# Optimization experiments

Hardware: AMD Instinct MI355X
Metric: run time of the kernel (lower is better)

The kernel has to match this reference:

```python
import jax, jax.numpy as jnp
import numpy as np

B, S, H = 2, 2048, 2048
NH = 16
Q_LORA = 1536
KV_LORA = 512
NOPE = 128
ROPE = 64
QHD = NOPE + ROPE  # 192
VHD = 128
FF = 8192
EPS = 1e-6
THETA = 10000.0


def rmsnorm(x, w, eps=EPS):
    var = jnp.mean(jnp.square(x), axis=-1, keepdims=True)
    return w * (x * jax.lax.rsqrt(var + eps))


def rotate_half(x):
    x1 = x[..., : x.shape[-1] // 2]
    x2 = x[..., x.shape[-1] // 2 :]
    return jnp.concatenate((-x2, x1), axis=-1)


def _deinterleave(x):
    # torch: x.view(b,h,s,d//2,2).transpose(0,1,2,4,3).reshape(b,h,s,d)
    b, h, s, d = x.shape
    return x.reshape(b, h, s, d // 2, 2).transpose(0, 1, 2, 4, 3).reshape(b, h, s, d)


def setup_inputs() -> dict:
    key = jax.random.key(0)
    ks = jax.random.split(key, 16)
    sc = 0.02
    # RoPE tables [S, ROPE]
    inv_freq = 1.0 / (THETA ** (np.arange(0, ROPE, 2, dtype=np.float64) / ROPE))
    freqs = np.outer(np.arange(S, dtype=np.float64), inv_freq)
    emb = np.concatenate([freqs, freqs], axis=-1)
    pos = jnp.sort(jax.random.randint(ks[15], (B, S), 0, S), axis=-1)
    return {
        "hidden_states": jax.random.normal(ks[0], (B, S, H), jnp.float32),
        "ln1_w": jnp.ones((H,), jnp.float32),
        "q_a_kernel": jax.random.normal(ks[1], (H, Q_LORA), jnp.float32) * sc,
        "q_a_ln_w": jnp.ones((Q_LORA,), jnp.float32),
        "q_b_kernel": jax.random.normal(ks[2], (Q_LORA, NH * QHD), jnp.float32) * sc,
        "kv_a_kernel": jax.random.normal(ks[3], (H, KV_LORA + ROPE), jnp.float32) * sc,
        "kv_a_ln_w": jnp.ones((KV_LORA,), jnp.float32),
        "kv_b_kernel": jax.random.normal(ks[4], (KV_LORA, NH * (NOPE + VHD)), jnp.float32) * sc,
        "o_kernel": jax.random.normal(ks[5], (NH * VHD, H), jnp.float32) * sc,
        "ln2_w": jnp.ones((H,), jnp.float32),
        "gate_kernel": jax.random.normal(ks[6], (H, FF), jnp.float32) * sc,
        "up_kernel": jax.random.normal(ks[7], (H, FF), jnp.float32) * sc,
        "down_kernel": jax.random.normal(ks[8], (FF, H), jnp.float32) * sc,
        "sin": jnp.asarray(np.sin(emb), jnp.float32),
        "cos": jnp.asarray(np.cos(emb), jnp.float32),
        "position_ids": pos,
    }


def reference(hidden_states, ln1_w, q_a_kernel, q_a_ln_w, q_b_kernel,
              kv_a_kernel, kv_a_ln_w, kv_b_kernel, o_kernel, ln2_w,
              gate_kernel, up_kernel, down_kernel, sin, cos, position_ids):
    b, s, h = hidden_states.shape
    x = rmsnorm(hidden_states, ln1_w)

    # --- MLA attention ---
    q = rmsnorm(x @ q_a_kernel, q_a_ln_w) @ q_b_kernel        # [b,s,NH*QHD]
    q = q.reshape(b, s, NH, QHD).transpose(0, 2, 1, 3)        # [b,NH,s,QHD]
    q_nope, q_pe = q[..., :NOPE], q[..., NOPE:]

    ckv = x @ kv_a_kernel                                     # [b,s,KV_LORA+ROPE]
    k_pe = ckv[..., KV_LORA:].reshape(b, s, 1, ROPE).transpose(0, 2, 1, 3)  # [b,1,s,ROPE]
    kv = rmsnorm(ckv[..., :KV_LORA], kv_a_ln_w) @ kv_b_kernel
    kv = kv.reshape(b, s, NH, NOPE + VHD).transpose(0, 2, 1, 3)
    k_nope = kv[..., :NOPE]
    v = kv[..., NOPE:]                                        # [b,NH,s,VHD]

    cos_e = cos[position_ids][:, None]                        # [b,1,s,ROPE]
    sin_e = sin[position_ids][:, None]
    q_pe = _deinterleave(q_pe)
    k_pe = _deinterleave(k_pe)
    q_pe = q_pe * cos_e + rotate_half(q_pe) * sin_e
    k_pe = k_pe * cos_e + rotate_half(k_pe) * sin_e

    qs = jnp.concatenate([q_nope, q_pe], axis=-1)             # [b,NH,s,QHD]
    ks = jnp.concatenate([k_nope, jnp.broadcast_to(k_pe, (b, NH, s, ROPE))], axis=-1)

    scale = QHD ** -0.5
    scores = jnp.einsum("bhqd,bhkd->bhqk", qs, ks) * scale
    causal = jnp.tril(jnp.ones((s, s), dtype=bool))
    scores = jnp.where(causal, scores, jnp.finfo(scores.dtype).min)
    probs = jax.nn.softmax(scores, axis=-1)
    attn = jnp.einsum("bhqk,bhkd->bhqd", probs, v)            # [b,NH,s,VHD]
    attn = attn.transpose(0, 2, 1, 3).reshape(b, s, NH * VHD)
    attn_out = attn @ o_kernel

    h1 = hidden_states + attn_out

    # --- dense MLP (SwiGLU) ---
    x2 = rmsnorm(h1, ln2_w)
    mlp = (jax.nn.silu(x2 @ gate_kernel) * (x2 @ up_kernel)) @ down_kernel
    return h1 + mlp
```

## Files before the change

kernel.cpp:

```cpp
#include <hip/hip_runtime.h>
#include <hip/hip_bf16.h>
#include <cstdint>

#define B_ 2
#define S_ 2048
#define H_ 2048
#define NH_ 16
#define QL_ 1536
#define KVL_ 512
#define NOPE_ 128
#define ROPE_ 64
#define QHD_ 192
#define VHD_ 128
#define FF_ 8192
#define BS_ (B_ * S_)
#define CKVP_ 640
#define KVW_ (NOPE_ + VHD_)

typedef __hip_bfloat16 bf16;
typedef __attribute__((ext_vector_type(8))) short short8_t;
typedef __attribute__((ext_vector_type(4))) float f32x4;

__device__ __forceinline__ float ldf(const float* p, size_t i) { return p[i]; }
__device__ __forceinline__ float ldf(const bf16* p, size_t i) { return __bfloat162float(p[i]); }
__device__ __forceinline__ void stf(float* p, size_t i, float v) { p[i] = v; }
__device__ __forceinline__ void stf(bf16* p, size_t i, float v) { p[i] = __float2bfloat16(v); }

__device__ __forceinline__ void gload16(const void* g, void* l)
{
    __builtin_amdgcn_global_load_lds((const unsigned int*)g, (unsigned int*)l, 16, 0, 0);
}

__global__ __launch_bounds__(256) void transp_bf16(
    const float* __restrict__ in, bf16* __restrict__ out, int K, int N, int Npad)
{
    __shared__ float t[32][33];
    const int n0 = blockIdx.x * 32, k0 = blockIdx.y * 32;
    for (int r = threadIdx.y; r < 32; r += 8) {
        const int n = n0 + threadIdx.x;
        t[r][threadIdx.x] = (n < N) ? in[(size_t)(k0 + r) * N + n] : 0.f;
    }
    __syncthreads();
    for (int r = threadIdx.y; r < 32; r += 8) {
        out[(size_t)(n0 + r) * K + k0 + threadIdx.x] = __float2bfloat16(t[threadIdx.x][r]);
    }
}

template<typename InT, typename OutT>
__global__ __launch_bounds__(256) void rmsnorm2(
    const InT* __restrict__ in, const float* __restrict__ w,
    OutT* __restrict__ out, int cols, int istride, int ostride)
{
    const int row = blockIdx.x;
    const InT* ip = in + (size_t)row * istride;
    OutT* op = out + (size_t)row * ostride;

    float ss = 0.f;
    for (int c = threadIdx.x; c < cols; c += 256) {
        float v = ldf(ip, c);
        ss = fmaf(v, v, ss);
    }
    #pragma unroll
    for (int off = 32; off; off >>= 1) ss += __shfl_xor(ss, off);
    __shared__ float red[4];
    if ((threadIdx.x & 63) == 0) red[threadIdx.x >> 6] = ss;
    __syncthreads();
    const float total = red[0] + red[1] + red[2] + red[3];
    const float scale = rsqrtf(total / (float)cols + 1e-6f);
    for (int c = threadIdx.x; c < cols; c += 256) {
        stf(op, c, ldf(ip, c) * scale * w[c]);
    }
}

template<int MODE, typename OutT>
__global__ __launch_bounds__(256) void gemm_bf16(
    const bf16* __restrict__ A, const bf16* __restrict__ BT,
    const float* __restrict__ Df, const bf16* __restrict__ Db,
    OutT* __restrict__ C, int M, int N, int K)
{
    __shared__ short As[128 * 32];
    __shared__ short Bs[128 * 32];
    const int tid = threadIdx.x;
    const int wid = tid >> 6, lane = tid & 63;
    const int bm = blockIdx.y * 128, bn = blockIdx.x * 128;
    const int wr = (wid >> 1) * 64, wc = (wid & 1) * 64;
    const int l16 = lane & 15;
    const int lk = (lane >> 4) << 3;

    f32x4 acc[4][4] = {};

    for (int k0 = 0; k0 < K; k0 += 32) {
        #pragma unroll
        for (int is = 0; is < 2; ++is) {
            const int c = is * 256 + tid;
            const int row = c >> 2;
            const int cb = (c & 3) * 16;
            const char* srcA = (const char*)A + ((size_t)(bm + row) * K + k0) * 2 + cb;
            const char* srcB = (const char*)BT + ((size_t)(bn + row) * K + k0) * 2 + cb;
            char* dstA = (char*)As + (is * 256 + wid * 64) * 16;
            char* dstB = (char*)Bs + (is * 256 + wid * 64) * 16;
            gload16(srcA, dstA);
            gload16(srcB, dstB);
        }
        __syncthreads();

        short8_t a[4], b[4];
        const short* ApW = As + (wr + l16) * 32 + lk;
        const short* BpW = Bs + (wc + l16) * 32 + lk;
        #pragma unroll
        for (int m = 0; m < 4; ++m) a[m] = *(const short8_t*)(ApW + m * 16 * 32);
        #pragma unroll
        for (int n = 0; n < 4; ++n) b[n] = *(const short8_t*)(BpW + n * 16 * 32);
        #pragma unroll
        for (int m = 0; m < 4; ++m)
            #pragma unroll
            for (int n = 0; n < 4; ++n)
                acc[m][n] = __builtin_amdgcn_mfma_f32_16x16x32_bf16(a[m], b[n], acc[m][n], 0, 0, 0);
        __syncthreads();
    }

    const int r0 = bm + wr + ((lane >> 4) << 2);
    const int c0 = bn + wc + l16;
    #pragma unroll
    for (int m = 0; m < 4; ++m) {
        #pragma unroll
        for (int n = 0; n < 4; ++n) {
            const int row = r0 + m * 16;
            const int col = c0 + n * 16;
            #pragma unroll
            for (int r = 0; r < 4; ++r) {
                const size_t off = (size_t)(row + r) * N + col;
                float v = acc[m][n][r];
                if (MODE == 1) v += Df[off];
                if (MODE == 2) {
                    const float g = __bfloat162float(Db[off]);
                    v *= g / (1.f + __expf(-g));
                }
                stf(C, off, v);
            }
        }
    }
}

__device__ __forceinline__ short8_t ldsfrag(const short* half_base, int r, int c)
{
    return *(const short8_t*)(half_base + r * 64 + ((c ^ (r & 7)) << 3));
}

template<int MODE, typename OutT>
__global__ __launch_bounds__(512, 2) void gemm256(
    const bf16* __restrict__ A, const bf16* __restrict__ BT,
    const float* __restrict__ Df, const bf16* __restrict__ Db,
    OutT* __restrict__ C, int M, int N, int K)
{
    __shared__ short lds[2][2][2][128 * 64];

    const int tid = threadIdx.x;
    const int wid = tid >> 6, lane = tid & 63;
    const int wm = wid >> 2, wn = wid & 3;
    const int l16 = lane & 15, hk = lane >> 4;

    const int nwg = gridDim.x * gridDim.y;
    const int orig = blockIdx.y * gridDim.x + blockIdx.x;
    const int q = nwg >> 3, r8 = nwg & 7;
    const int xcd = orig & 7, lid = orig >> 3;
    const int wg = (xcd < r8 ? xcd * (q + 1) : r8 * (q + 1) + (xcd - r8) * q) + lid;
    const int bn = (wg % gridDim.x) * 256;
    const int bm = (wg / gridDim.x) * 256;

    f32x4 acc[8][4] = {};

    const int nt = K >> 6;

    auto stage_half = [&](const bf16* gbase, int ldk, short* lbase) {
        #pragma unroll
        for (int i = 0; i < 2; ++i) {
            const int ch = i * 512 + tid;
            const int row = ch >> 3, pc = ch & 7;
            const int gc = pc ^ (row & 7);
            const char* src = (const char*)(gbase + (size_t)row * ldk + gc * 8);
            char* dst = (char*)lbase + (i * 512 + wid * 64) * 16;
            gload16(src, dst);
        }
    };

    stage_half(A + (size_t)bm * K, K, &lds[0][0][0][0]);
    stage_half(A + (size_t)(bm + 128) * K, K, &lds[0][0][1][0]);
    stage_half(BT + (size_t)bn * K, K, &lds[0][1][0][0]);
    stage_half(BT + (size_t)(bn + 128) * K, K, &lds[0][1][1][0]);
    asm volatile("s_waitcnt vmcnt(0)" ::: "memory");
    __syncthreads();

    int cur = 0;
    for (int t = 0; t < nt; ++t) {
        const int k0n = (t + 1) << 6;
        const short* Ah = &lds[cur][0][wm][0];
        const short* Bh = &lds[cur][1][wn >> 1][0];
        const int brr = (wn & 1) * 64;

        short8_t bfr[4][2], afr[2][2];

        #pragma unroll
        for (int nf = 0; nf < 4; ++nf)
            #pragma unroll
            for (int ks = 0; ks < 2; ++ks)
                bfr[nf][ks] = ldsfrag(Bh, brr + nf * 16 + l16, ks * 4 + hk);
        #pragma unroll
        for (int mi = 0; mi < 2; ++mi)
            #pragma unroll
            for (int ks = 0; ks < 2; ++ks)
                afr[mi][ks] = ldsfrag(Ah, mi * 16 + l16, ks * 4 + hk);
        if (t + 1 < nt) {
            stage_half(A + (size_t)bm * K + k0n, K, &lds[cur ^ 1][0][0][0]);
            stage_half(A + (size_t)(bm + 128) * K + k0n, K, &lds[cur ^ 1][0][1][0]);
        }
        __builtin_amdgcn_s_barrier();
        __builtin_amdgcn_s_setprio(1);
        #pragma unroll
        for (int mi = 0; mi < 2; ++mi)
            #pragma unroll
            for (int nf = 0; nf < 4; ++nf)
                #pragma unroll
                for (int ks = 0; ks < 2; ++ks)
                    acc[mi][nf] = __builtin_amdgcn_mfma_f32_16x16x32_bf16(
                        afr[mi][ks], bfr[nf][ks], acc[mi][nf], 0, 0, 0);
        __builtin_amdgcn_s_setprio(0);
        __builtin_amdgcn_s_barrier();

        #pragma unroll
        for (int mi = 0; mi < 2; ++mi)
            #pragma unroll
            for (int ks = 0; ks < 2; ++ks)
                afr[mi][ks] = ldsfrag(Ah, 32 + mi * 16 + l16, ks * 4 + hk);
        if (t + 1 < nt) {
            stage_half(BT + (size_t)bn * K + k0n, K, &lds[cur ^ 1][1][0][0]);
            stage_half(BT + (size_t)(bn + 128) * K + k0n, K, &lds[cur ^ 1][1][1][0]);
        }
        __builtin_amdgcn_s_barrier();
        __builtin_amdgcn_s_setprio(1);
        #pragma unroll
        for (int mi = 0; mi < 2; ++mi)
            #pragma unroll
            for (int nf = 0; nf < 4; ++nf)
                #pragma unroll
                for (int ks = 0; ks < 2; ++ks)
                    acc[2 + mi][nf] = __builtin_amdgcn_mfma_f32_16x16x32_bf16(
                        afr[mi][ks], bfr[nf][ks], acc[2 + mi][nf], 0, 0, 0);
        __builtin_amdgcn_s_setprio(0);
        __builtin_amdgcn_s_barrier();

        #pragma unroll
        for (int mi = 0; mi < 2; ++mi)
            #pragma unroll
            for (int ks = 0; ks < 2; ++ks)
                afr[mi][ks] = ldsfrag(Ah, 64 + mi * 16 + l16, ks * 4 + hk);
        __builtin_amdgcn_s_barrier();
        __builtin_amdgcn_s_setprio(1);
        #pragma unroll
        for (int mi = 0; mi < 2; ++mi)
            #pragma unroll
            for (int nf = 0; nf < 4; ++nf)
                #pragma unroll
                for (int ks = 0; ks < 2; ++ks)
                    acc[4 + mi][nf] = __builtin_amdgcn_mfma_f32_16x16x32_bf16(
                        afr[mi][ks], bfr[nf][ks], acc[4 + mi][nf], 0, 0, 0);
        __builtin_amdgcn_s_setprio(0);
        __builtin_amdgcn_s_barrier();

        #pragma unroll
        for (int mi = 0; mi < 2; ++mi)
            #pragma unroll
            for (int ks = 0; ks < 2; ++ks)
                afr[mi][ks] = ldsfrag(Ah, 96 + mi * 16 + l16, ks * 4 + hk);
        __builtin_amdgcn_s_barrier();
        __builtin_amdgcn_s_setprio(1);
        #pragma unroll
        for (int mi = 0; mi < 2; ++mi)
            #pragma unroll
            for (int nf = 0; nf < 4; ++nf)
                #pragma unroll
                for (int ks = 0; ks < 2; ++ks)
                    acc[6 + mi][nf] = __builtin_amdgcn_mfma_f32_16x16x32_bf16(
                        afr[mi][ks], bfr[nf][ks], acc[6 + mi][nf], 0, 0, 0);
        __builtin_amdgcn_s_setprio(0);
        asm volatile("s_waitcnt vmcnt(0)" ::: "memory");
        __syncthreads();
        cur ^= 1;
    }

    const int r0 = bm + wm * 128 + (lane >> 4) * 4;
    const int c0 = bn + wn * 64 + l16;
    #pragma unroll
    for (int mf = 0; mf < 8; ++mf) {
        #pragma unroll
        for (int nf = 0; nf < 4; ++nf) {
            const int row = r0 + mf * 16;
            const int col = c0 + nf * 16;
            #pragma unroll
            for (int r = 0; r < 4; ++r) {
                const size_t off = (size_t)(row + r) * N + col;
                float v = acc[mf][nf][r];
                if (MODE == 1) v += Df[off];
                if (MODE == 2) {
                    const float g = __bfloat162float(Db[off]);
                    v *= g / (1.f + __expf(-g));
                }
                stf(C, off, v);
            }
        }
    }
}

__global__ __launch_bounds__(256) void rope_kernel(
    bf16* __restrict__ q, float* __restrict__ ckv,
    const int* __restrict__ pos_ids,
    const float* __restrict__ sinT, const float* __restrict__ cosT)
{
    const int wid = blockIdx.x * 4 + (threadIdx.x >> 6);
    const int lane = threadIdx.x & 63;
    const int NQ = BS_ * NH_;

    int bs;
    bf16* bptr = nullptr;
    float* fptr = nullptr;
    if (wid < NQ) {
        bs = wid >> 4;
        bptr = q + (size_t)wid * QHD_ + NOPE_;
    } else {
        bs = wid - NQ;
        fptr = ckv + (size_t)bs * CKVP_ + KVL_;
    }
    const int pos = pos_ids[bs];
    const float c  = cosT[pos * ROPE_ + lane];
    const float sn = sinT[pos * ROPE_ + lane];
    const float x = bptr ? __bfloat162float(bptr[lane]) : fptr[lane];
    const int j = lane & 31;
    const float x0 = __shfl(x, 2 * j);
    const float x1 = __shfl(x, 2 * j + 1);
    const float res = (lane < 32) ? fmaf(x0, c, -x1 * sn) : fmaf(x1, c, x0 * sn);
    if (bptr) bptr[lane] = __float2bfloat16(res);
    else      fptr[lane] = res;
}

__global__ __launch_bounds__(256) void pack_k(
    const float* __restrict__ KV, const float* __restrict__ CKV,
    bf16* __restrict__ Kh)
{
    const int total = BS_ * NH_ * (QHD_ / 2);
    for (int i = blockIdx.x * 256 + threadIdx.x; i < total; i += gridDim.x * 256) {
        const int d2 = i % (QHD_ / 2);
        const int t  = i / (QHD_ / 2);
        const int s  = t % S_;
        const int hh = (t / S_) % NH_;
        const int bb = t / (S_ * NH_);
        const int d = d2 * 2;
        float2 v;
        if (d < NOPE_) v = *(const float2*)&KV[(((size_t)bb * S_ + s) * NH_ + hh) * KVW_ + d];
        else           v = *(const float2*)&CKV[((size_t)bb * S_ + s) * CKVP_ + KVL_ + (d - NOPE_)];
        union { bf16 h[2]; unsigned int u; } cv;
        cv.h[0] = __float2bfloat16(v.x);
        cv.h[1] = __float2bfloat16(v.y);
        *(unsigned int*)&Kh[((size_t)(bb * NH_ + hh) * S_ + s) * QHD_ + d] = cv.u;
    }
}

__global__ __launch_bounds__(256) void pack_vt(
    const float* __restrict__ KV, bf16* __restrict__ Vt)
{
    __shared__ float t[32][33];
    const int s0 = blockIdx.x * 32, d0 = blockIdx.y * 32;
    const int bh = blockIdx.z;
    const int tx = threadIdx.x & 31, ty = threadIdx.x >> 5;
    for (int r = ty; r < 32; r += 8)
        t[r][tx] = KV[(((size_t)(bh >> 4) * S_ + s0 + r) * NH_ + (bh & 15)) * KVW_ + NOPE_ + d0 + tx];
    __syncthreads();
    for (int r = ty; r < 32; r += 8)
        Vt[((size_t)bh * VHD_ + d0 + r) * S_ + s0 + tx] = __float2bfloat16(t[tx][r]);
}

__global__ __launch_bounds__(512, 2) void attn_mfma(
    const bf16* __restrict__ Qp, const bf16* __restrict__ Kh,
    const bf16* __restrict__ Vt, bf16* __restrict__ outp)
{
    __shared__ __align__(16) short Ks[64][192];
    __shared__ __align__(16) short Vs[128][64];
    __shared__ __align__(16) short Ps[8][16][64];

    const int tid = threadIdx.x;
    const int wid = tid >> 6, lane = tid & 63;
    const int l16 = lane & 15;
    const int hk  = lane >> 4;
    const int lk  = hk << 3;
    const int pr  = hk << 2;
    const int lx  = l16 & 7;

    const int bid = blockIdx.x;
    const int orig = (bid & 7) * 64 + (bid >> 3);
    const int j  = orig & 15;
    const int gh = orig >> 4;
    const int h = gh & 15, b = gh >> 4;

    const int setB = wid >> 2;
    const int qblk = setB ? (31 - j) : j;
    const int qw = qblk * 64 + (wid & 3) * 16;
    const int myNt = qblk + 1;
    const int ntStage = 32 - j;

    short8_t qf[6];
    const bf16* qbase = Qp + (((size_t)b * S_ + qw + l16) * NH_ + h) * QHD_;
    #pragma unroll
    for (int kk = 0; kk < 6; ++kk)
        qf[kk] = *(const short8_t*)(qbase + kk * 32 + lk);

    const bf16* Khb = Kh + (size_t)(b * NH_ + h) * S_ * QHD_;
    const bf16* Vtb = Vt + (size_t)(b * NH_ + h) * VHD_ * S_;

    f32x4 o[8] = {};
    float mr[4] = {-3.0e38f, -3.0e38f, -3.0e38f, -3.0e38f};
    float lr[4] = {0.f, 0.f, 0.f, 0.f};
    const float scale = 0.07216878364870323f;

    const int krow = tid >> 3, kc0 = (tid & 7) * 3;
    const int vrow = tid >> 2, vc0 = (tid & 3) * 2;

    short8_t kreg[3], vreg[2];
    auto load_tile = [&](int kt) {
        const short* ksrc = (const short*)(Khb + ((size_t)(kt * 64 + krow)) * QHD_);
        kreg[0] = *(const short8_t*)(ksrc + (kc0 + 0) * 8);
        kreg[1] = *(const short8_t*)(ksrc + (kc0 + 1) * 8);
        kreg[2] = *(const short8_t*)(ksrc + (kc0 + 2) * 8);
        const short* vsrc = (const short*)(Vtb + (size_t)vrow * S_ + kt * 64);
        vreg[0] = *(const short8_t*)(vsrc + (vc0 + 0) * 8);
        vreg[1] = *(const short8_t*)(vsrc + (vc0 + 1) * 8);
    };
    auto write_tile = [&]() {
        const int kx = krow & 7, vx = vrow & 7;
        *(short8_t*)&Ks[krow][((kc0 + 0) ^ kx) << 3] = kreg[0];
        *(short8_t*)&Ks[krow][((kc0 + 1) ^ kx) << 3] = kreg[1];
        *(short8_t*)&Ks[krow][((kc0 + 2) ^ kx) << 3] = kreg[2];
        *(short8_t*)&Vs[vrow][((vc0 + 0) ^ vx) << 3] = vreg[0];
        *(short8_t*)&Vs[vrow][((vc0 + 1) ^ vx) << 3] = vreg[1];
    };

    load_tile(0);

    for (int t = 0; t < ntStage; ++t) {
        write_tile();
        __syncthreads();
        if (t + 1 < ntStage) load_tile(t + 1);
        if (t < myNt) {
            const int k0 = t << 6;
            f32x4 s[4] = {};
            #pragma unroll
            for (int kk = 0; kk < 6; ++kk) {
                #pragma unroll
                for (int n = 0; n < 4; ++n) {
                    short8_t kf = *(const short8_t*)&Ks[n * 16 + l16][((kk * 4 + hk) ^ lx) << 3];
                    s[n] = __builtin_amdgcn_mfma_f32_16x16x32_bf16(qf[kk], kf, s[n], 0, 0, 0);
                }
            }
            if (t == myNt - 1) {
                #pragma unroll
                for (int n = 0; n < 4; ++n) {
                    const int kg = k0 + n * 16 + l16;
                    #pragma unroll
                    for (int r = 0; r < 4; ++r) {
                        if (kg > qw + pr + r) s[n][r] = -3.0e38f;
                    }
                }
            }
            #pragma unroll
            for (int r = 0; r < 4; ++r) {
                float rm = fmaxf(fmaxf(s[0][r], s[1][r]), fmaxf(s[2][r], s[3][r]));
                rm = fmaxf(rm, __shfl_xor(rm, 1));
                rm = fmaxf(rm, __shfl_xor(rm, 2));
                rm = fmaxf(rm, __shfl_xor(rm, 4));
                rm = fmaxf(rm, __shfl_xor(rm, 8));
                const float mnew = fmaxf(mr[r], rm);
                const float corr = __expf((mr[r] - mnew) * scale);
                mr[r] = mnew;
                float rs = 0.f;
                #pragma unroll
                for (int n = 0; n < 4; ++n) {
                    const float p = __expf((s[n][r] - mnew) * scale);
                    s[n][r] = p;
                    rs += p;
                }
                rs += __shfl_xor(rs, 1);
                rs += __shfl_xor(rs, 2);
                rs += __shfl_xor(rs, 4);
                rs += __shfl_xor(rs, 8);
                lr[r] = lr[r] * corr + rs;
                #pragma unroll
                for (int n = 0; n < 8; ++n) o[n][r] *= corr;
            }
            #pragma unroll
            for (int n = 0; n < 4; ++n) {
                #pragma unroll
                for (int r = 0; r < 4; ++r) {
                    union { bf16 hh; short u; } cv;
                    cv.hh = __float2bfloat16(s[n][r]);
                    const int row = pr + r;
                    const int col = (((n * 2 + (l16 >> 3)) ^ (row & 7)) << 3) + (l16 & 7);
                    Ps[wid][row][col] = cv.u;
                }
            }
            #pragma unroll
            for (int kk2 = 0; kk2 < 2; ++kk2) {
                short8_t pf = *(const short8_t*)&Ps[wid][l16][((kk2 * 4 + hk) ^ lx) << 3];
                #pragma unroll
                for (int n = 0; n < 8; ++n) {
                    short8_t vf = *(const short8_t*)&Vs[n * 16 + l16][((kk2 * 4 + hk) ^ lx) << 3];
                    o[n] = __builtin_amdgcn_mfma_f32_16x16x32_bf16(pf, vf, o[n], 0, 0, 0);
                }
            }
        }
        __syncthreads();
    }

    float inv[4];
    #pragma unroll
    for (int r = 0; r < 4; ++r) inv[r] = 1.f / lr[r];
    bf16* ob = outp + (((size_t)b * S_ + qw + pr) * NH_ + h) * VHD_;
    #pragma unroll
    for (int r = 0; r < 4; ++r)
        #pragma unroll
        for (int n = 0; n < 8; ++n)
            ob[(size_t)r * (NH_ * VHD_) + n * 16 + l16] = __float2bfloat16(o[n][r] * inv[r]);
}

extern "C" void kernel_launch(void* const* d_in, const int* in_sizes, int n_in,
                              void* d_out, int out_size, void* d_ws, size_t ws_size,
                              hipStream_t stream)
{
    const float* hidden  = (const float*)d_in[0];
    const float* ln1_w   = (const float*)d_in[1];
    const float* q_a_k   = (const float*)d_in[2];
    const float* q_a_ln  = (const float*)d_in[3];
    const float* q_b_k   = (const float*)d_in[4];
    const float* kv_a_k  = (const float*)d_in[5];
    const float* kv_a_ln = (const float*)d_in[6];
    const float* kv_b_k  = (const float*)d_in[7];
    const float* o_k     = (const float*)d_in[8];
    const float* ln2_w   = (const float*)d_in[9];
    const float* gate_k  = (const float*)d_in[10];
    const float* up_k    = (const float*)d_in[11];
    const float* down_k  = (const float*)d_in[12];
    const float* sinT    = (const float*)d_in[13];
    const float* cosT    = (const float*)d_in[14];
    const int*   pos     = (const int*)d_in[15];
    float* out = (float*)d_out;
    char* ws = (char*)d_ws;

    bf16* qaT   = (bf16*)(ws + 0);
    bf16* qbT   = (bf16*)(ws + 6291456);
    bf16* kvaT  = (bf16*)(ws + 15728640);
    bf16* kvbT  = (bf16*)(ws + 18350080);
    bf16* oT    = (bf16*)(ws + 22544384);
    bf16* Xb    = (bf16*)(ws + 30932992);
    bf16* QAb   = (bf16*)(ws + 47710208);
    bf16* CKVNb = (bf16*)(ws + 60293120);
    bf16* Qb    = (bf16*)(ws + 64487424);
    float* CKV  = (float*)(ws + 89653248);
    float* KV   = (float*)(ws + 100139008);
    bf16* ATTNb = (bf16*)(ws + 167247872);
    bf16* Vt    = (bf16*)(ws + 0);
    bf16* Kh    = (bf16*)(ws + 30932992);
    bf16* gateT = (bf16*)(ws + 0);
    bf16* upT   = (bf16*)(ws + 33554432);
    bf16* downT = (bf16*)(ws + 67108864);
    bf16* X2b   = (bf16*)(ws + 100663296);
    bf16* MLPb  = (bf16*)(ws + 117440512);

    const dim3 tb(32, 8);

    transp_bf16<<<dim3(1536 / 32, 2048 / 32), tb, 0, stream>>>(q_a_k, qaT, 2048, 1536, 1536);
    transp_bf16<<<dim3(3072 / 32, 1536 / 32), tb, 0, stream>>>(q_b_k, qbT, 1536, 3072, 3072);
    transp_bf16<<<dim3(640 / 32, 2048 / 32), tb, 0, stream>>>(kv_a_k, kvaT, 2048, 576, 640);
    transp_bf16<<<dim3(4096 / 32, 512 / 32), tb, 0, stream>>>(kv_b_k, kvbT, 512, 4096, 4096);
    transp_bf16<<<dim3(2048 / 32, 2048 / 32), tb, 0, stream>>>(o_k, oT, 2048, 2048, 2048);

    rmsnorm2<float, bf16><<<BS_, 256, 0, stream>>>(hidden, ln1_w, Xb, H_, H_, H_);
    gemm_bf16<0, bf16><<<dim3(QL_ / 128, BS_ / 128), 256, 0, stream>>>(
        Xb, qaT, nullptr, nullptr, QAb, BS_, QL_, H_);
    rmsnorm2<bf16, bf16><<<BS_, 256, 0, stream>>>(QAb, q_a_ln, QAb, QL_, QL_, QL_);
    gemm256<0, bf16><<<dim3((NH_ * QHD_) / 256, BS_ / 256), 512, 0, stream>>>(
        QAb, qbT, nullptr, nullptr, Qb, BS_, NH_ * QHD_, QL_);
    gemm_bf16<0, float><<<dim3(CKVP_ / 128, BS_ / 128), 256, 0, stream>>>(
        Xb, kvaT, nullptr, nullptr, CKV, BS_, CKVP_, H_);
    rmsnorm2<float, bf16><<<BS_, 256, 0, stream>>>(CKV, kv_a_ln, CKVNb, KVL_, CKVP_, KVL_);
    gemm256<0, float><<<dim3((NH_ * KVW_) / 256, BS_ / 256), 512, 0, stream>>>(
        CKVNb, kvbT, nullptr, nullptr, KV, BS_, NH_ * KVW_, KVL_);
    rope_kernel<<<(BS_ * NH_ + BS_) / 4, 256, 0, stream>>>(Qb, CKV, pos, sinT, cosT);
    pack_k<<<2048, 256, 0, stream>>>(KV, CKV, Kh);
    pack_vt<<<dim3(S_ / 32, VHD_ / 32, B_ * NH_), 256, 0, stream>>>(KV, Vt);
    attn_mfma<<<dim3(512), 512, 0, stream>>>(Qb, Kh, Vt, ATTNb);
    gemm256<1, float><<<dim3(H_ / 256, BS_ / 256), 512, 0, stream>>>(
        ATTNb, oT, hidden, nullptr, out, BS_, H_, NH_ * VHD_);

    transp_bf16<<<dim3(8192 / 32, 2048 / 32), tb, 0, stream>>>(gate_k, gateT, 2048, 8192, 8192);
    transp_bf16<<<dim3(8192 / 32, 2048 / 32), tb, 0, stream>>>(up_k, upT, 2048, 8192, 8192);
    transp_bf16<<<dim3(2048 / 32, 8192 / 32), tb, 0, stream>>>(down_k, downT, 8192, 2048, 2048);

    rmsnorm2<float, bf16><<<BS_, 256, 0, stream>>>(out, ln2_w, X2b, H_, H_, H_);
    gemm256<0, bf16><<<dim3(FF_ / 256, BS_ / 256), 512, 0, stream>>>(
        X2b, gateT, nullptr, nullptr, MLPb, BS_, FF_, H_);
    gemm256<2, bf16><<<dim3(FF_ / 256, BS_ / 256), 512, 0, stream>>>(
        X2b, upT, nullptr, MLPb, MLPb, BS_, FF_, H_);
    gemm256<1, float><<<dim3(H_ / 256, BS_ / 256), 512, 0, stream>>>(
        MLPb, downT, out, nullptr, out, BS_, H_, FF_);
}
```

Before: 1.071 ms.

## Prefetch two K-tiles ahead in gemm256 and add 256x128 tile variant for narrow GEMMs

The 256x256 GEMM now issues loads for tile t+2 into the buffer just consumed, waiting with a partial vmcnt so one tile is always in flight, instead of splitting the next tile's loads across the first two compute phases and draining with a full syncthreads. A new 256x128-tile kernel with the same pipeline is used for the q_b, o-projection and down-projection GEMMs, whose N of 2048-3072 gives few workgroups at 256x256 tiles. This doubles the grid for those GEMMs to improve CU occupancy, at the cost of lower arithmetic intensity per tile.

```diff
diff --git a/kernel.cpp b/kernel.cpp
--- a/kernel.cpp
+++ b/kernel.cpp
@@ -142,6 +142,20 @@
     }
 }
 
+template<int MODE, typename OutT>
+__device__ __forceinline__ void epi_store(
+    OutT* __restrict__ C, const float* __restrict__ Df, const bf16* __restrict__ Db,
+    int N, int row, int col, float v)
+{
+    const size_t off = (size_t)row * N + col;
+    if (MODE == 1) v += Df[off];
+    if (MODE == 2) {
+        const float g = __bfloat162float(Db[off]);
+        v *= g / (1.f + __expf(-g));
+    }
+    stf(C, off, v);
+}
+
 __device__ __forceinline__ short8_t ldsfrag(const short* half_base, int r, int c)
 {
     return *(const short8_t*)(half_base + r * 64 + ((c ^ (r & 7)) << 3));
@@ -169,31 +183,34 @@
     const int bm = (wg / gridDim.x) * 256;
 
     f32x4 acc[8][4] = {};
-
     const int nt = K >> 6;
 
-    auto stage_half = [&](const bf16* gbase, int ldk, short* lbase) {
+    auto stage_half = [&](const bf16* gbase, short* lbase) {
         #pragma unroll
         for (int i = 0; i < 2; ++i) {
             const int ch = i * 512 + tid;
             const int row = ch >> 3, pc = ch & 7;
             const int gc = pc ^ (row & 7);
-            const char* src = (const char*)(gbase + (size_t)row * ldk + gc * 8);
+            const char* src = (const char*)(gbase + (size_t)row * K + gc * 8);
             char* dst = (char*)lbase + (i * 512 + wid * 64) * 16;
             gload16(src, dst);
         }
     };
-
-    stage_half(A + (size_t)bm * K, K, &lds[0][0][0][0]);
-    stage_half(A + (size_t)(bm + 128) * K, K, &lds[0][0][1][0]);
-    stage_half(BT + (size_t)bn * K, K, &lds[0][1][0][0]);
-    stage_half(BT + (size_t)(bn + 128) * K, K, &lds[0][1][1][0]);
-    asm volatile("s_waitcnt vmcnt(0)" ::: "memory");
-    __syncthreads();
+    auto stage_tile = [&](int t, int buf) {
+        const int k0 = t << 6;
+        stage_half(A + (size_t)bm * K + k0,          &lds[buf][0][0][0]);
+        stage_half(A + (size_t)(bm + 128) * K + k0,  &lds[buf][0][1][0]);
+        stage_half(BT + (size_t)bn * K + k0,         &lds[buf][1][0][0]);
+        stage_half(BT + (size_t)(bn + 128) * K + k0, &lds[buf][1][1][0]);
+    };
+
+    stage_tile(0, 0);
+    stage_tile(1, 1);
+    asm volatile("s_waitcnt vmcnt(8)" ::: "memory");
+    __builtin_amdgcn_s_barrier();
 
     int cur = 0;
     for (int t = 0; t < nt; ++t) {
-        const int k0n = (t + 1) << 6;
         const short* Ah = &lds[cur][0][wm][0];
         const short* Bh = &lds[cur][1][wn >> 1][0];
         const int brr = (wn & 1) * 64;
@@ -210,10 +227,6 @@
             #pragma unroll
             for (int ks = 0; ks < 2; ++ks)
                 afr[mi][ks] = ldsfrag(Ah, mi * 16 + l16, ks * 4 + hk);
-        if (t + 1 < nt) {
-            stage_half(A + (size_t)bm * K + k0n, K, &lds[cur ^ 1][0][0][0]);
-            stage_half(A + (size_t)(bm + 128) * K + k0n, K, &lds[cur ^ 1][0][1][0]);
-        }
         __builtin_amdgcn_s_barrier();
         __builtin_amdgcn_s_setprio(1);
         #pragma unroll
@@ -228,14 +241,131 @@
         __builtin_amdgcn_s_barrier();
 
         #pragma unroll
+        for (int ph = 1; ph < 4; ++ph) {
+            #pragma unroll
+            for (int mi = 0; mi < 2; ++mi)
+                #pragma unroll
+                for (int ks = 0; ks < 2; ++ks)
+                    afr[mi][ks] = ldsfrag(Ah, ph * 32 + mi * 16 + l16, ks * 4 + hk);
+            __builtin_amdgcn_s_barrier();
+            __builtin_amdgcn_s_setprio(1);
+            #pragma unroll
+            for (int mi = 0; mi < 2; ++mi)
+                #pragma unroll
+                for (int nf = 0; nf < 4; ++nf)
+                    #pragma unroll
+                    for (int ks = 0; ks < 2; ++ks)
+                        acc[ph * 2 + mi][nf] = __builtin_amdgcn_mfma_f32_16x16x32_bf16(
+                            afr[mi][ks], bfr[nf][ks], acc[ph * 2 + mi][nf], 0, 0, 0);
+            __builtin_amdgcn_s_setprio(0);
+            __builtin_amdgcn_s_barrier();
+        }
+
+        if (t + 2 < nt) {
+            stage_tile(t + 2, cur);
+            asm volatile("s_waitcnt vmcnt(8)" ::: "memory");
+        } else if (t + 1 < nt) {
+            asm volatile("s_waitcnt vmcnt(0)" ::: "memory");
+        }
+        __builtin_amdgcn_s_barrier();
+        cur ^= 1;
+    }
+
+    const int r0 = bm + wm * 128 + (lane >> 4) * 4;
+    const int c0 = bn + wn * 64 + l16;
+    #pragma unroll
+    for (int mf = 0; mf < 8; ++mf)
+        #pragma unroll
+        for (int nf = 0; nf < 4; ++nf)
+            #pragma unroll
+            for (int r = 0; r < 4; ++r)
+                epi_store<MODE>(C, Df, Db, N, r0 + mf * 16 + r, c0 + nf * 16, acc[mf][nf][r]);
+}
+
+template<int MODE, typename OutT>
+__global__ __launch_bounds__(512, 2) void gemm256n128(
+    const bf16* __restrict__ A, const bf16* __restrict__ BT,
+    const float* __restrict__ Df, const bf16* __restrict__ Db,
+    OutT* __restrict__ C, int M, int N, int K)
+{
+    __shared__ short lds[2][3][128 * 64];
+
+    const int tid = threadIdx.x;
+    const int wid = tid >> 6, lane = tid & 63;
+    const int wm = wid >> 1, wn = wid & 1;
+    const int l16 = lane & 15, hk = lane >> 4;
+
+    const int nwg = gridDim.x * gridDim.y;
+    const int orig = blockIdx.y * gridDim.x + blockIdx.x;
+    const int q = nwg >> 3, r8 = nwg & 7;
+    const int xcd = orig & 7, lid = orig >> 3;
+    const int wg = (xcd < r8 ? xcd * (q + 1) : r8 * (q + 1) + (xcd - r8) * q) + lid;
+    const int bn = (wg % gridDim.x) * 128;
+    const int bm = (wg / gridDim.x) * 256;
+
+    f32x4 acc[4][4] = {};
+    const int nt = K >> 6;
+
+    auto stage_half = [&](const bf16* gbase, short* lbase) {
+        #pragma unroll
+        for (int i = 0; i < 2; ++i) {
+            const int ch = i * 512 + tid;
+            const int row = ch >> 3, pc = ch & 7;
+            const int gc = pc ^ (row & 7);
+            const char* src = (const char*)(gbase + (size_t)row * K + gc * 8);
+            char* dst = (char*)lbase + (i * 512 + wid * 64) * 16;
+            gload16(src, dst);
+        }
+    };
+    auto stage_tile = [&](int t, int buf) {
+        const int k0 = t << 6;
+        stage_half(A + (size_t)bm * K + k0,          &lds[buf][0][0]);
+        stage_half(A + (size_t)(bm + 128) * K + k0,  &lds[buf][1][0]);
+        stage_half(BT + (size_t)bn * K + k0,         &lds[buf][2][0]);
+    };
+
+    stage_tile(0, 0);
+    stage_tile(1, 1);
+    asm volatile("s_waitcnt vmcnt(6)" ::: "memory");
+    __builtin_amdgcn_s_barrier();
+
+    int cur = 0;
+    for (int t = 0; t < nt; ++t) {
+        const short* Ah = &lds[cur][wm >> 1][0];
+        const short* Bh = &lds[cur][2][0];
+        const int arr = (wm & 1) * 64;
+        const int brr = wn * 64;
+
+        short8_t bfr[4][2], afr[2][2];
+
+        #pragma unroll
+        for (int nf = 0; nf < 4; ++nf)
+            #pragma unroll
+            for (int ks = 0; ks < 2; ++ks)
+                bfr[nf][ks] = ldsfrag(Bh, brr + nf * 16 + l16, ks * 4 + hk);
+        #pragma unroll
         for (int mi = 0; mi < 2; ++mi)
             #pragma unroll
             for (int ks = 0; ks < 2; ++ks)
-                afr[mi][ks] = ldsfrag(Ah, 32 + mi * 16 + l16, ks * 4 + hk);
-        if (t + 1 < nt) {
-            stage_half(BT + (size_t)bn * K + k0n, K, &lds[cur ^ 1][1][0][0]);
-            stage_half(BT + (size_t)(bn + 128) * K + k0n, K, &lds[cur ^ 1][1][1][0]);
-        }
+                afr[mi][ks] = ldsfrag(Ah, arr + mi * 16 + l16, ks * 4 + hk);
+        __builtin_amdgcn_s_barrier();
+        __builtin_amdgcn_s_setprio(1);
+        #pragma unroll
+        for (int mi = 0; mi < 2; ++mi)
+            #pragma unroll
+            for (int nf = 0; nf < 4; ++nf)
+                #pragma unroll
+                for (int ks = 0; ks < 2; ++ks)
+                    acc[mi][nf] = __builtin_amdgcn_mfma_f32_16x16x32_bf16(
+                        afr[mi][ks], bfr[nf][ks], acc[mi][nf], 0, 0, 0);
+        __builtin_amdgcn_s_setprio(0);
+        __builtin_amdgcn_s_barrier();
+
+        #pragma unroll
+        for (int mi = 0; mi < 2; ++mi)
+            #pragma unroll
+            for (int ks = 0; ks < 2; ++ks)
+                afr[mi][ks] = ldsfrag(Ah, arr + 32 + mi * 16 + l16, ks * 4 + hk);
         __builtin_amdgcn_s_barrier();
         __builtin_amdgcn_s_setprio(1);
         #pragma unroll
@@ -249,66 +379,25 @@
         __builtin_amdgcn_s_setprio(0);
         __builtin_amdgcn_s_barrier();
 
-        #pragma unroll
-        for (int mi = 0; mi < 2; ++mi)
-            #pragma unroll
-            for (int ks = 0; ks < 2; ++ks)
-                afr[mi][ks] = ldsfrag(Ah, 64 + mi * 16 + l16, ks * 4 + hk);
+        if (t + 2 < nt) {
+            stage_tile(t + 2, cur);
+            asm volatile("s_waitcnt vmcnt(6)" ::: "memory");
+        } else if (t + 1 < nt) {
+            asm volatile("s_waitcnt vmcnt(0)" ::: "memory");
+        }
         __builtin_amdgcn_s_barrier();
-        __builtin_amdgcn_s_setprio(1);
-        #pragma unroll
-        for (int mi = 0; mi < 2; ++mi)
-            #pragma unroll
-            for (int nf = 0; nf < 4; ++nf)
-                #pragma unroll
-                for (int ks = 0; ks < 2; ++ks)
-                    acc[4 + mi][nf] = __builtin_amdgcn_mfma_f32_16x16x32_bf16(
-                        afr[mi][ks], bfr[nf][ks], acc[4 + mi][nf], 0, 0, 0);
-        __builtin_amdgcn_s_setprio(0);
-        __builtin_amdgcn_s_barrier();
-
-        #pragma unroll
-        for (int mi = 0; mi < 2; ++mi)
-            #pragma unroll
-            for (int ks = 0; ks < 2; ++ks)
-                afr[mi][ks] = ldsfrag(Ah, 96 + mi * 16 + l16, ks * 4 + hk);
-        __builtin_amdgcn_s_barrier();
-        __builtin_amdgcn_s_setprio(1);
-        #pragma unroll
-        for (int mi = 0; mi < 2; ++mi)
-            #pragma unroll
-            for (int nf = 0; nf < 4; ++nf)
-                #pragma unroll
-                for (int ks = 0; ks < 2; ++ks)
-                    acc[6 + mi][nf] = __builtin_amdgcn_mfma_f32_16x16x32_bf16(
-                        afr[mi][ks], bfr[nf][ks], acc[6 + mi][nf], 0, 0, 0);
-        __builtin_amdgcn_s_setprio(0);
-        asm volatile("s_waitcnt vmcnt(0)" ::: "memory");
-        __syncthreads();
         cur ^= 1;
     }
 
-    const int r0 = bm + wm * 128 + (lane >> 4) * 4;
+    const int r0 = bm + wm * 64 + (lane >> 4) * 4;
     const int c0 = bn + wn * 64 + l16;
     #pragma unroll
-    for (int mf = 0; mf < 8; ++mf) {
-        #pragma unroll
-        for (int nf = 0; nf < 4; ++nf) {
-            const int row = r0 + mf * 16;
-            const int col = c0 + nf * 16;
-            #pragma unroll
-            for (int r = 0; r < 4; ++r) {
-                const size_t off = (size_t)(row + r) * N + col;
-                float v = acc[mf][nf][r];
-                if (MODE == 1) v += Df[off];
-                if (MODE == 2) {
-                    const float g = __bfloat162float(Db[off]);
-                    v *= g / (1.f + __expf(-g));
-                }
-                stf(C, off, v);
-            }
-        }
-    }
+    for (int mf = 0; mf < 4; ++mf)
+        #pragma unroll
+        for (int nf = 0; nf < 4; ++nf)
+            #pragma unroll
+            for (int r = 0; r < 4; ++r)
+                epi_store<MODE>(C, Df, Db, N, r0 + mf * 16 + r, c0 + nf * 16, acc[mf][nf][r]);
 }
 
 __global__ __launch_bounds__(256) void rope_kernel(
@@ -584,7 +673,7 @@
     gemm_bf16<0, bf16><<<dim3(QL_ / 128, BS_ / 128), 256, 0, stream>>>(
         Xb, qaT, nullptr, nullptr, QAb, BS_, QL_, H_);
     rmsnorm2<bf16, bf16><<<BS_, 256, 0, stream>>>(QAb, q_a_ln, QAb, QL_, QL_, QL_);
-    gemm256<0, bf16><<<dim3((NH_ * QHD_) / 256, BS_ / 256), 512, 0, stream>>>(
+    gemm256n128<0, bf16><<<dim3((NH_ * QHD_) / 128, BS_ / 256), 512, 0, stream>>>(
         QAb, qbT, nullptr, nullptr, Qb, BS_, NH_ * QHD_, QL_);
     gemm_bf16<0, float><<<dim3(CKVP_ / 128, BS_ / 128), 256, 0, stream>>>(
         Xb, kvaT, nullptr, nullptr, CKV, BS_, CKVP_, H_);
@@ -595,7 +684,7 @@
     pack_k<<<2048, 256, 0, stream>>>(KV, CKV, Kh);
     pack_vt<<<dim3(S_ / 32, VHD_ / 32, B_ * NH_), 256, 0, stream>>>(KV, Vt);
     attn_mfma<<<dim3(512), 512, 0, stream>>>(Qb, Kh, Vt, ATTNb);
-    gemm256<1, float><<<dim3(H_ / 256, BS_ / 256), 512, 0, stream>>>(
+    gemm256n128<1, float><<<dim3(H_ / 128, BS_ / 256), 512, 0, stream>>>(
         ATTNb, oT, hidden, nullptr, out, BS_, H_, NH_ * VHD_);
 
     transp_bf16<<<dim3(8192 / 32, 2048 / 32), tb, 0, stream>>>(gate_k, gateT, 2048, 8192, 8192);
@@ -607,6 +696,6 @@
         X2b, gateT, nullptr, nullptr, MLPb, BS_, FF_, H_);
     gemm256<2, bf16><<<dim3(FF_ / 256, BS_ / 256), 512, 0, stream>>>(
         X2b, upT, nullptr, MLPb, MLPb, BS_, FF_, H_);
-    gemm256<1, float><<<dim3(H_ / 256, BS_ / 256), 512, 0, stream>>>(
+    gemm256n128<1, float><<<dim3(H_ / 128, BS_ / 256), 512, 0, stream>>>(
         MLPb, downT, out, nullptr, out, BS_, H_, FF_);
 }
```

After: 1.004 ms. -6.2%, faster.
